# Kernel tuning notes

Hardware: AMD Instinct MI355X
Metric: run time of the kernel (lower is better)

## Reference

```python
import jax, jax.numpy as jnp
import numpy as np

N = 8192
F = 128

def setup_inputs() -> dict:
    key = jax.random.key(0)
    k1, k2, k3 = jax.random.split(key, 3)
    x = jax.random.normal(k1, (N, F), dtype=jnp.float32)
    adj = jax.random.uniform(k2, (N, N), dtype=jnp.float32)
    # xavier-uniform style init for weight [F, F]
    limit = float(np.sqrt(6.0 / (F + F)))
    weight = jax.random.uniform(k3, (F, F), dtype=jnp.float32, minval=-limit, maxval=limit)
    return {"x": x, "adj": adj, "weight": weight}

def reference(x, adj, weight):
    # adj_hat = adj + I
    n = adj.shape[0]
    adj_hat = adj + jnp.eye(n, dtype=adj.dtype)
    # degree vector; D^{-1/2} A_hat D^{-1/2} expressed as row/col scaling
    deg = jnp.sum(adj_hat, axis=1)
    d_inv_sqrt = (deg + 1e-8) ** -0.5  # [N]
    support = d_inv_sqrt[:, None] * adj_hat * d_inv_sqrt[None, :]  # [N, N]
    out = jnp.matmul(jnp.matmul(support, x), weight)  # [N, F]
    return jax.nn.relu(out)
```

## Files before the change

### kernel.cpp

```cpp
#include <hip/hip_runtime.h>
#include <hip/hip_bf16.h>

#define NN 8192
#define FF 128
#define BM 64
#define BK 64
#define KS 8
#define KCH (NN / KS)
#define NSTEP (KCH / BK)

typedef __attribute__((ext_vector_type(8))) short bf16x8;
typedef __attribute__((ext_vector_type(4))) float f32x4;

__device__ __forceinline__ short f2bf(float f) {
  unsigned u = __float_as_uint(f);
  u += 0x7FFFu + ((u >> 16) & 1u);
  return (short)(u >> 16);
}
__device__ __forceinline__ float bf2f(short s) {
  return __uint_as_float(((unsigned)(unsigned short)s) << 16);
}

__global__ __launch_bounds__(256) void k_deg(const float* __restrict__ adj,
                                             float* __restrict__ dinv) {
  const int row = blockIdx.x;
  const float4* p = (const float4*)(adj + (size_t)row * NN);
  float s = 0.f;
#pragma unroll
  for (int it = 0; it < 8; ++it) {
    float4 v = p[it * 256 + threadIdx.x];
    s += (v.x + v.y) + (v.z + v.w);
  }
#pragma unroll
  for (int off = 32; off > 0; off >>= 1) s += __shfl_down(s, off, 64);
  __shared__ float partial[4];
  if ((threadIdx.x & 63) == 0) partial[threadIdx.x >> 6] = s;
  __syncthreads();
  if (threadIdx.x == 0) {
    float deg = (partial[0] + partial[1]) + (partial[2] + partial[3]) + 1.0f;
    dinv[row] = 1.0f / sqrtf(deg + 1e-8f);
  }
}

__global__ __launch_bounds__(256) void k_scale_t(const float* __restrict__ x,
                                                 const float* __restrict__ dinv,
                                                 short* __restrict__ yT) {
  __shared__ float tile[64][129];
  const int r0 = blockIdx.x * 64;
  const int tid = threadIdx.x;
#pragma unroll
  for (int it = 0; it < 8; ++it) {
    int q = it * 256 + tid;
    int r = q >> 5;
    int c = q & 31;
    float4 v = ((const float4*)(x + (size_t)(r0 + r) * FF))[c];
    float d = dinv[r0 + r];
    tile[r][c * 4 + 0] = v.x * d;
    tile[r][c * 4 + 1] = v.y * d;
    tile[r][c * 4 + 2] = v.z * d;
    tile[r][c * 4 + 3] = v.w * d;
  }
  __syncthreads();
  const int f = tid >> 1;
  const int i0 = (tid & 1) * 32;
#pragma unroll
  for (int g = 0; g < 4; ++g) {
    bf16x8 o;
#pragma unroll
    for (int j = 0; j < 8; ++j) o[j] = f2bf(tile[i0 + g * 8 + j][f]);
    *(bf16x8*)(yT + (size_t)f * NN + r0 + i0 + g * 8) = o;
  }
}

__global__ __launch_bounds__(512, 4) void k_gemm(const float* __restrict__ adj,
                                                 const short* __restrict__ yT,
                                                 short* __restrict__ zpart) {
  __shared__ short As[2][BM][72];
  __shared__ short Bs[2][128][72];
  const int tid = threadIdx.x;
  const int wave = tid >> 6;
  const int lane = tid & 63;
  const int mb = 127 - (int)(blockIdx.x & 127);
  const int ks = blockIdx.x >> 7;
  const int row0 = mb * BM;
  const size_t kbase = (size_t)ks * KCH;

  const int s_ar = tid >> 3;
  const int s_ac = (tid & 7) * 8;
  const float* pa  = adj + (size_t)(row0 + s_ar) * NN + kbase + s_ac;
  const short* pb0 = yT + (size_t)s_ar * NN + kbase + s_ac;
  const short* pb1 = yT + (size_t)(s_ar + 64) * NN + kbase + s_ac;

  const int wm = (wave >> 2) * 32;
  const int wn = (wave & 3) * 32;
  const int fr = lane & 15;
  const int kh = (lane >> 4) * 8;

  f32x4 acc00 = {0.f,0.f,0.f,0.f}, acc01 = acc00, acc10 = acc00, acc11 = acc00;

  float4 aXlo, aXhi, aYlo, aYhi;
  bf16x8 bX0, bX1, bY0, bY1;

#define LOADT(alo, ahi, b0v, b1v, koff) do {                                   \
    alo = *(const float4*)(pa + (koff));                                       \
    ahi = *(const float4*)(pa + (koff) + 4);                                   \
    b0v = *(const bf16x8*)(pb0 + (koff));                                      \
    b1v = *(const bf16x8*)(pb1 + (koff));                                      \
  } while (0)

#define STAGE(BUF, alo, ahi, b0v, b1v) do {                                    \
    bf16x8 ap_;                                                                \
    ap_[0] = f2bf(alo.x); ap_[1] = f2bf(alo.y);                                \
    ap_[2] = f2bf(alo.z); ap_[3] = f2bf(alo.w);                                \
    ap_[4] = f2bf(ahi.x); ap_[5] = f2bf(ahi.y);                                \
    ap_[6] = f2bf(ahi.z); ap_[7] = f2bf(ahi.w);                                \
    *(bf16x8*)&As[BUF][s_ar][s_ac] = ap_;                                      \
    *(bf16x8*)&Bs[BUF][s_ar][s_ac] = b0v;                                      \
    *(bf16x8*)&Bs[BUF][s_ar + 64][s_ac] = b1v;                                 \
  } while (0)

#define COMPUTE(BUF) do {                                                      \
    _Pragma("unroll")                                                          \
    for (int kk = 0; kk < 2; ++kk) {                                           \
      bf16x8 a0 = *(const bf16x8*)&As[BUF][wm + fr][kk * 32 + kh];             \
      bf16x8 a1 = *(const bf16x8*)&As[BUF][wm + 16 + fr][kk * 32 + kh];        \
      bf16x8 b0 = *(const bf16x8*)&Bs[BUF][wn + fr][kk * 32 + kh];             \
      bf16x8 b1 = *(const bf16x8*)&Bs[BUF][wn + 16 + fr][kk * 32 + kh];        \
      acc00 = __builtin_amdgcn_mfma_f32_16x16x32_bf16(a0, b0, acc00, 0, 0, 0); \
      acc01 = __builtin_amdgcn_mfma_f32_16x16x32_bf16(a0, b1, acc01, 0, 0, 0); \
      acc10 = __builtin_amdgcn_mfma_f32_16x16x32_bf16(a1, b0, acc10, 0, 0, 0); \
      acc11 = __builtin_amdgcn_mfma_f32_16x16x32_bf16(a1, b1, acc11, 0, 0, 0); \
    }                                                                          \
  } while (0)

  LOADT(aXlo, aXhi, bX0, bX1, 0);
  LOADT(aYlo, aYhi, bY0, bY1, BK);
  STAGE(0, aXlo, aXhi, bX0, bX1);
  __syncthreads();

  for (int step = 0; step < NSTEP; step += 2) {
    STAGE(1, aYlo, aYhi, bY0, bY1);
    if (step + 2 < NSTEP) LOADT(aXlo, aXhi, bX0, bX1, (step + 2) * BK);
    COMPUTE(0);
    __syncthreads();
    if (step + 2 < NSTEP) STAGE(0, aXlo, aXhi, bX0, bX1);
    if (step + 3 < NSTEP) LOADT(aYlo, aYhi, bY0, bY1, (step + 3) * BK);
    COMPUTE(1);
    __syncthreads();
  }

  const int r4 = (lane >> 4) * 4;
  short* zp = zpart + ((size_t)ks << 20);
#pragma unroll
  for (int r = 0; r < 4; ++r) {
    int gi0 = row0 + wm + r4 + r;
    int gi1 = gi0 + 16;
    zp[(size_t)gi0 * FF + wn + fr]      = f2bf(acc00[r]);
    zp[(size_t)gi0 * FF + wn + 16 + fr] = f2bf(acc01[r]);
    zp[(size_t)gi1 * FF + wn + fr]      = f2bf(acc10[r]);
    zp[(size_t)gi1 * FF + wn + 16 + fr] = f2bf(acc11[r]);
  }
#undef LOADT
#undef STAGE
#undef COMPUTE
}

__global__ __launch_bounds__(256) void k_out(const short* __restrict__ zpart,
                                             const float* __restrict__ x,
                                             const float* __restrict__ dinv,
                                             const float* __restrict__ w,
                                             float* __restrict__ out) {
  __shared__ float zs[16][128];
  const int r0 = blockIdx.x * 16;
  const int tid = threadIdx.x;
#pragma unroll
  for (int half = 0; half < 2; ++half) {
    int p = half * 256 + tid;
    int r = p >> 5;
    int c4 = p & 31;
    int gi = r0 + r;
    const short* base = zpart + (size_t)gi * FF + c4 * 4;
    float s0 = 0.f, s1 = 0.f, s2 = 0.f, s3 = 0.f;
#pragma unroll
    for (int sidx = 0; sidx < KS; ++sidx) {
      short4 v = *(const short4*)(base + ((size_t)sidx << 20));
      s0 += bf2f(v.x); s1 += bf2f(v.y); s2 += bf2f(v.z); s3 += bf2f(v.w);
    }
    float4 xv = *(const float4*)(x + (size_t)gi * FF + c4 * 4);
    float di = dinv[gi];
    float di2 = di * di;
    zs[r][c4 * 4 + 0] = di * s0 + di2 * xv.x;
    zs[r][c4 * 4 + 1] = di * s1 + di2 * xv.y;
    zs[r][c4 * 4 + 2] = di * s2 + di2 * xv.z;
    zs[r][c4 * 4 + 3] = di * s3 + di2 * xv.w;
  }
  __syncthreads();
  const int f = tid & 127;
  const int rg = (tid >> 7) * 8;
  float acc[8] = {0.f, 0.f, 0.f, 0.f, 0.f, 0.f, 0.f, 0.f};
#pragma unroll 4
  for (int k = 0; k < 128; ++k) {
    float wv = w[k * FF + f];
#pragma unroll
    for (int r = 0; r < 8; ++r) acc[r] += zs[rg + r][k] * wv;
  }
#pragma unroll
  for (int r = 0; r < 8; ++r) {
    out[(size_t)(r0 + rg + r) * FF + f] = fmaxf(acc[r], 0.0f);
  }
}

extern "C" void kernel_launch(void* const* d_in, const int* in_sizes, int n_in,
                              void* d_out, int out_size, void* d_ws, size_t ws_size,
                              hipStream_t stream) {
  const float* x   = (const float*)d_in[0];
  const float* adj = (const float*)d_in[1];
  const float* w   = (const float*)d_in[2];
  float* out = (float*)d_out;

  float* dinv  = (float*)d_ws;
  short* yT    = (short*)((char*)d_ws + 64 * 1024);
  short* zpart = (short*)((char*)d_ws + 4 * 1024 * 1024);

  k_deg    <<<NN,      256, 0, stream>>>(adj, dinv);
  k_scale_t<<<NN / 64, 256, 0, stream>>>(x, dinv, yT);
  k_gemm   <<<128 * KS, 512, 0, stream>>>(adj, yT, zpart);
  k_out    <<<NN / 16, 256, 0, stream>>>(zpart, x, dinv, w, out);
}
```

Baseline: 114.4 us.

## Double GEMM M-tile and load B operand directly into registers

The main GEMM now uses 128-row tiles, so each wave computes a 64x32 output with eight accumulators, and the grid shrinks to 512 blocks. The B operand (the scaled transposed features) is no longer staged through shared memory. Each wave loads its MFMA fragments straight from global memory into registers, double-buffered across steps. This halves the number of times the bf16 feature matrix is re-read per row block and removes the B shared-memory traffic. In exchange it costs more registers per thread, fewer blocks for the 256-CU device to occupy, and uncoalesced per-lane B loads.

```diff
diff --git a/kernel.cpp b/kernel.cpp
--- a/kernel.cpp
+++ b/kernel.cpp
@@ -3,7 +3,7 @@
 
 #define NN 8192
 #define FF 128
-#define BM 64
+#define BM 128
 #define BK 64
 #define KS 8
 #define KCH (NN / KS)
@@ -76,91 +76,115 @@
                                                  const short* __restrict__ yT,
                                                  short* __restrict__ zpart) {
   __shared__ short As[2][BM][72];
-  __shared__ short Bs[2][128][72];
   const int tid = threadIdx.x;
   const int wave = tid >> 6;
   const int lane = tid & 63;
-  const int mb = 127 - (int)(blockIdx.x & 127);
-  const int ks = blockIdx.x >> 7;
+  const int mb = 63 - (int)(blockIdx.x & 63);
+  const int ks = blockIdx.x >> 6;
   const int row0 = mb * BM;
   const size_t kbase = (size_t)ks * KCH;
 
-  const int s_ar = tid >> 3;
-  const int s_ac = (tid & 7) * 8;
-  const float* pa  = adj + (size_t)(row0 + s_ar) * NN + kbase + s_ac;
-  const short* pb0 = yT + (size_t)s_ar * NN + kbase + s_ac;
-  const short* pb1 = yT + (size_t)(s_ar + 64) * NN + kbase + s_ac;
-
-  const int wm = (wave >> 2) * 32;
+  const int s_ar = tid >> 2;
+  const int s_ac = (tid & 3) * 16;
+  const float* pa = adj + (size_t)(row0 + s_ar) * NN + kbase + s_ac;
+
+  const int wm = (wave >> 2) * 64;
   const int wn = (wave & 3) * 32;
   const int fr = lane & 15;
   const int kh = (lane >> 4) * 8;
 
+  const short* pb0 = yT + (size_t)(wn + fr) * NN + kbase + kh;
+  const short* pb1 = pb0 + (size_t)16 * NN;
+
   f32x4 acc00 = {0.f,0.f,0.f,0.f}, acc01 = acc00, acc10 = acc00, acc11 = acc00;
-
-  float4 aXlo, aXhi, aYlo, aYhi;
-  bf16x8 bX0, bX1, bY0, bY1;
-
-#define LOADT(alo, ahi, b0v, b1v, koff) do {                                   \
-    alo = *(const float4*)(pa + (koff));                                       \
-    ahi = *(const float4*)(pa + (koff) + 4);                                   \
-    b0v = *(const bf16x8*)(pb0 + (koff));                                      \
-    b1v = *(const bf16x8*)(pb1 + (koff));                                      \
-  } while (0)
-
-#define STAGE(BUF, alo, ahi, b0v, b1v) do {                                    \
-    bf16x8 ap_;                                                                \
-    ap_[0] = f2bf(alo.x); ap_[1] = f2bf(alo.y);                                \
-    ap_[2] = f2bf(alo.z); ap_[3] = f2bf(alo.w);                                \
-    ap_[4] = f2bf(ahi.x); ap_[5] = f2bf(ahi.y);                                \
-    ap_[6] = f2bf(ahi.z); ap_[7] = f2bf(ahi.w);                                \
-    *(bf16x8*)&As[BUF][s_ar][s_ac] = ap_;                                      \
-    *(bf16x8*)&Bs[BUF][s_ar][s_ac] = b0v;                                      \
-    *(bf16x8*)&Bs[BUF][s_ar + 64][s_ac] = b1v;                                 \
-  } while (0)
-
-#define COMPUTE(BUF) do {                                                      \
+  f32x4 acc20 = acc00, acc21 = acc00, acc30 = acc00, acc31 = acc00;
+
+  float4 aR0, aR1, aR2, aR3;
+  bf16x8 bX[4], bY[4];
+
+#define LOADA(koff) do {                                                       \
+    aR0 = *(const float4*)(pa + (koff));                                       \
+    aR1 = *(const float4*)(pa + (koff) + 4);                                   \
+    aR2 = *(const float4*)(pa + (koff) + 8);                                   \
+    aR3 = *(const float4*)(pa + (koff) + 12);                                  \
+  } while (0)
+
+#define LOADB(dst, koff) do {                                                  \
+    dst[0] = *(const bf16x8*)(pb0 + (koff));                                   \
+    dst[1] = *(const bf16x8*)(pb0 + (koff) + 32);                              \
+    dst[2] = *(const bf16x8*)(pb1 + (koff));                                   \
+    dst[3] = *(const bf16x8*)(pb1 + (koff) + 32);                              \
+  } while (0)
+
+#define STAGE(BUF) do {                                                        \
+    bf16x8 lo_, hi_;                                                           \
+    lo_[0] = f2bf(aR0.x); lo_[1] = f2bf(aR0.y);                                \
+    lo_[2] = f2bf(aR0.z); lo_[3] = f2bf(aR0.w);                                \
+    lo_[4] = f2bf(aR1.x); lo_[5] = f2bf(aR1.y);                                \
+    lo_[6] = f2bf(aR1.z); lo_[7] = f2bf(aR1.w);                                \
+    hi_[0] = f2bf(aR2.x); hi_[1] = f2bf(aR2.y);                                \
+    hi_[2] = f2bf(aR2.z); hi_[3] = f2bf(aR2.w);                                \
+    hi_[4] = f2bf(aR3.x); hi_[5] = f2bf(aR3.y);                                \
+    hi_[6] = f2bf(aR3.z); hi_[7] = f2bf(aR3.w);                                \
+    *(bf16x8*)&As[BUF][s_ar][s_ac]     = lo_;                                  \
+    *(bf16x8*)&As[BUF][s_ar][s_ac + 8] = hi_;                                  \
+  } while (0)
+
+#define COMPUTE(BUF, breg) do {                                                \
     _Pragma("unroll")                                                          \
     for (int kk = 0; kk < 2; ++kk) {                                           \
-      bf16x8 a0 = *(const bf16x8*)&As[BUF][wm + fr][kk * 32 + kh];             \
+      bf16x8 a0 = *(const bf16x8*)&As[BUF][wm +  0 + fr][kk * 32 + kh];        \
       bf16x8 a1 = *(const bf16x8*)&As[BUF][wm + 16 + fr][kk * 32 + kh];        \
-      bf16x8 b0 = *(const bf16x8*)&Bs[BUF][wn + fr][kk * 32 + kh];             \
-      bf16x8 b1 = *(const bf16x8*)&Bs[BUF][wn + 16 + fr][kk * 32 + kh];        \
-      acc00 = __builtin_amdgcn_mfma_f32_16x16x32_bf16(a0, b0, acc00, 0, 0, 0); \
-      acc01 = __builtin_amdgcn_mfma_f32_16x16x32_bf16(a0, b1, acc01, 0, 0, 0); \
-      acc10 = __builtin_amdgcn_mfma_f32_16x16x32_bf16(a1, b0, acc10, 0, 0, 0); \
-      acc11 = __builtin_amdgcn_mfma_f32_16x16x32_bf16(a1, b1, acc11, 0, 0, 0); \
+      bf16x8 a2 = *(const bf16x8*)&As[BUF][wm + 32 + fr][kk * 32 + kh];        \
+      bf16x8 a3 = *(const bf16x8*)&As[BUF][wm + 48 + fr][kk * 32 + kh];        \
+      acc00 = __builtin_amdgcn_mfma_f32_16x16x32_bf16(a0, breg[kk],     acc00, 0, 0, 0); \
+      acc01 = __builtin_amdgcn_mfma_f32_16x16x32_bf16(a0, breg[2 + kk], acc01, 0, 0, 0); \
+      acc10 = __builtin_amdgcn_mfma_f32_16x16x32_bf16(a1, breg[kk],     acc10, 0, 0, 0); \
+      acc11 = __builtin_amdgcn_mfma_f32_16x16x32_bf16(a1, breg[2 + kk], acc11, 0, 0, 0); \
+      acc20 = __builtin_amdgcn_mfma_f32_16x16x32_bf16(a2, breg[kk],     acc20, 0, 0, 0); \
+      acc21 = __builtin_amdgcn_mfma_f32_16x16x32_bf16(a2, breg[2 + kk], acc21, 0, 0, 0); \
+      acc30 = __builtin_amdgcn_mfma_f32_16x16x32_bf16(a3, breg[kk],     acc30, 0, 0, 0); \
+      acc31 = __builtin_amdgcn_mfma_f32_16x16x32_bf16(a3, breg[2 + kk], acc31, 0, 0, 0); \
     }                                                                          \
   } while (0)
 
-  LOADT(aXlo, aXhi, bX0, bX1, 0);
-  LOADT(aYlo, aYhi, bY0, bY1, BK);
-  STAGE(0, aXlo, aXhi, bX0, bX1);
+  LOADA(0);
+  STAGE(0);
+  LOADA(BK);
+  LOADB(bX, 0);
+  LOADB(bY, BK);
   __syncthreads();
 
   for (int step = 0; step < NSTEP; step += 2) {
-    STAGE(1, aYlo, aYhi, bY0, bY1);
-    if (step + 2 < NSTEP) LOADT(aXlo, aXhi, bX0, bX1, (step + 2) * BK);
-    COMPUTE(0);
+    if (step + 1 < NSTEP) STAGE(1);
+    if (step + 2 < NSTEP) LOADA((step + 2) * BK);
+    COMPUTE(0, bX);
+    if (step + 2 < NSTEP) LOADB(bX, (step + 2) * BK);
     __syncthreads();
-    if (step + 2 < NSTEP) STAGE(0, aXlo, aXhi, bX0, bX1);
-    if (step + 3 < NSTEP) LOADT(aYlo, aYhi, bY0, bY1, (step + 3) * BK);
-    COMPUTE(1);
+    if (step + 2 < NSTEP) STAGE(0);
+    if (step + 3 < NSTEP) LOADA((step + 3) * BK);
+    COMPUTE(1, bY);
+    if (step + 3 < NSTEP) LOADB(bY, (step + 3) * BK);
     __syncthreads();
   }
 
   const int r4 = (lane >> 4) * 4;
   short* zp = zpart + ((size_t)ks << 20);
-#pragma unroll
-  for (int r = 0; r < 4; ++r) {
-    int gi0 = row0 + wm + r4 + r;
-    int gi1 = gi0 + 16;
-    zp[(size_t)gi0 * FF + wn + fr]      = f2bf(acc00[r]);
-    zp[(size_t)gi0 * FF + wn + 16 + fr] = f2bf(acc01[r]);
-    zp[(size_t)gi1 * FF + wn + fr]      = f2bf(acc10[r]);
-    zp[(size_t)gi1 * FF + wn + 16 + fr] = f2bf(acc11[r]);
-  }
-#undef LOADT
+#define STOREM(accn0, accn1, MOFF) do {                                        \
+    _Pragma("unroll")                                                          \
+    for (int r = 0; r < 4; ++r) {                                              \
+      int gi = row0 + wm + (MOFF) + r4 + r;                                    \
+      zp[(size_t)gi * FF + wn + fr]      = f2bf(accn0[r]);                     \
+      zp[(size_t)gi * FF + wn + 16 + fr] = f2bf(accn1[r]);                     \
+    }                                                                          \
+  } while (0)
+  STOREM(acc00, acc01, 0);
+  STOREM(acc10, acc11, 16);
+  STOREM(acc20, acc21, 32);
+  STOREM(acc30, acc31, 48);
+#undef STOREM
+#undef LOADA
+#undef LOADB
 #undef STAGE
 #undef COMPUTE
 }
@@ -224,6 +248,6 @@
 
   k_deg    <<<NN,      256, 0, stream>>>(adj, dinv);
   k_scale_t<<<NN / 64, 256, 0, stream>>>(x, dinv, yT);
-  k_gemm   <<<128 * KS, 512, 0, stream>>>(adj, yT, zpart);
+  k_gemm   <<<64 * KS, 512, 0, stream>>>(adj, yT, zpart);
   k_out    <<<NN / 16, 256, 0, stream>>>(zpart, x, dinv, w, out);
 }
```

After: 120.6 us. +5.5%, slower.

## Stage GEMM tiles via direct global-to-LDS DMA with XOR swizzle

Applied to the files above, without the earlier changes.

The GEMM kernel now loads adjacency (fp32) and yT tiles straight from global memory into LDS with global_load_lds, so staging no longer passes through registers. A uses an XOR-swizzled layout to avoid bank conflicts. The fp32-to-bf16 conversion moves from staging to the compute phase and uses packed v_cvt_pk_bf16_f32. The fp32 A tile doubles LDS usage and the conversion is repeated by every wave that reads the tile; the occupancy hint in launch_bounds is also removed.

```diff
diff --git a/kernel.cpp b/kernel.cpp
--- a/kernel.cpp
+++ b/kernel.cpp
@@ -19,6 +19,22 @@
 }
 __device__ __forceinline__ float bf2f(short s) {
   return __uint_as_float(((unsigned)(unsigned short)s) << 16);
+}
+
+__device__ __forceinline__ void dma16(const void* g, void* lds) {
+  __builtin_amdgcn_global_load_lds(
+      (const __attribute__((address_space(1))) unsigned int*)(uintptr_t)g,
+      (__attribute__((address_space(3))) unsigned int*)(lds),
+      16, 0, 0);
+}
+
+__device__ __forceinline__ bf16x8 cvt8(float4 lo, float4 hi) {
+  union { bf16x8 v; unsigned u[4]; } r;
+  asm("v_cvt_pk_bf16_f32 %0, %1, %2" : "=v"(r.u[0]) : "v"(lo.x), "v"(lo.y));
+  asm("v_cvt_pk_bf16_f32 %0, %1, %2" : "=v"(r.u[1]) : "v"(lo.z), "v"(lo.w));
+  asm("v_cvt_pk_bf16_f32 %0, %1, %2" : "=v"(r.u[2]) : "v"(hi.x), "v"(hi.y));
+  asm("v_cvt_pk_bf16_f32 %0, %1, %2" : "=v"(r.u[3]) : "v"(hi.z), "v"(hi.w));
+  return r.v;
 }
 
 __global__ __launch_bounds__(256) void k_deg(const float* __restrict__ adj,
@@ -72,11 +88,11 @@
   }
 }
 
-__global__ __launch_bounds__(512, 4) void k_gemm(const float* __restrict__ adj,
-                                                 const short* __restrict__ yT,
-                                                 short* __restrict__ zpart) {
-  __shared__ short As[2][BM][72];
-  __shared__ short Bs[2][128][72];
+__global__ __launch_bounds__(512) void k_gemm(const float* __restrict__ adj,
+                                              const short* __restrict__ yT,
+                                              short* __restrict__ zpart) {
+  __shared__ float Asf[2][BM * BK];
+  __shared__ short Bsf[2][128 * BK];
   const int tid = threadIdx.x;
   const int wave = tid >> 6;
   const int lane = tid & 63;
@@ -85,47 +101,53 @@
   const int row0 = mb * BM;
   const size_t kbase = (size_t)ks * KCH;
 
-  const int s_ar = tid >> 3;
-  const int s_ac = (tid & 7) * 8;
-  const float* pa  = adj + (size_t)(row0 + s_ar) * NN + kbase + s_ac;
-  const short* pb0 = yT + (size_t)s_ar * NN + kbase + s_ac;
-  const short* pb1 = yT + (size_t)(s_ar + 64) * NN + kbase + s_ac;
+  const int rowA = tid >> 4;
+  const int c4l  = (tid & 15) ^ (rowA & 7);
+  const float* pa0 = adj + (size_t)(row0 + rowA) * NN + kbase + c4l * 4;
+  const float* pa1 = pa0 + (size_t)32 * NN;
+  const int rowB = tid >> 3;
+  const int c8l  = (tid & 7) ^ (rowB & 7);
+  const short* pb0 = yT + (size_t)rowB * NN + kbase + c8l * 8;
+  const short* pb1 = pb0 + (size_t)64 * NN;
+
+  const int ldsOff = wave * 1024;
+
+#define STAGE_DMA(BUF, koff) do {                                              \
+    char* la = (char*)&Asf[BUF][0] + ldsOff;                                   \
+    char* lb = (char*)&Bsf[BUF][0] + ldsOff;                                   \
+    dma16(pa0 + (koff), la);                                                   \
+    dma16(pa1 + (koff), la + 8192);                                            \
+    dma16(pb0 + (koff), lb);                                                   \
+    dma16(pb1 + (koff), lb + 8192);                                            \
+  } while (0)
 
   const int wm = (wave >> 2) * 32;
   const int wn = (wave & 3) * 32;
   const int fr = lane & 15;
   const int kh = (lane >> 4) * 8;
+  const int khq = kh >> 2;
+  const int kh8 = kh >> 3;
+  const int sw  = fr & 7;
+  const int ra0 = wm + fr, ra1 = ra0 + 16;
+  const int rb0 = wn + fr, rb1 = rb0 + 16;
 
   f32x4 acc00 = {0.f,0.f,0.f,0.f}, acc01 = acc00, acc10 = acc00, acc11 = acc00;
 
-  float4 aXlo, aXhi, aYlo, aYhi;
-  bf16x8 bX0, bX1, bY0, bY1;
-
-#define LOADT(alo, ahi, b0v, b1v, koff) do {                                   \
-    alo = *(const float4*)(pa + (koff));                                       \
-    ahi = *(const float4*)(pa + (koff) + 4);                                   \
-    b0v = *(const bf16x8*)(pb0 + (koff));                                      \
-    b1v = *(const bf16x8*)(pb1 + (koff));                                      \
-  } while (0)
-
-#define STAGE(BUF, alo, ahi, b0v, b1v) do {                                    \
-    bf16x8 ap_;                                                                \
-    ap_[0] = f2bf(alo.x); ap_[1] = f2bf(alo.y);                                \
-    ap_[2] = f2bf(alo.z); ap_[3] = f2bf(alo.w);                                \
-    ap_[4] = f2bf(ahi.x); ap_[5] = f2bf(ahi.y);                                \
-    ap_[6] = f2bf(ahi.z); ap_[7] = f2bf(ahi.w);                                \
-    *(bf16x8*)&As[BUF][s_ar][s_ac] = ap_;                                      \
-    *(bf16x8*)&Bs[BUF][s_ar][s_ac] = b0v;                                      \
-    *(bf16x8*)&Bs[BUF][s_ar + 64][s_ac] = b1v;                                 \
-  } while (0)
-
 #define COMPUTE(BUF) do {                                                      \
+    const char* Ab = (const char*)&Asf[BUF][0];                                \
+    const char* Bb = (const char*)&Bsf[BUF][0];                                \
     _Pragma("unroll")                                                          \
     for (int kk = 0; kk < 2; ++kk) {                                           \
-      bf16x8 a0 = *(const bf16x8*)&As[BUF][wm + fr][kk * 32 + kh];             \
-      bf16x8 a1 = *(const bf16x8*)&As[BUF][wm + 16 + fr][kk * 32 + kh];        \
-      bf16x8 b0 = *(const bf16x8*)&Bs[BUF][wn + fr][kk * 32 + kh];             \
-      bf16x8 b1 = *(const bf16x8*)&Bs[BUF][wn + 16 + fr][kk * 32 + kh];        \
+      int c4 = kk * 8 + khq;                                                   \
+      int c8 = kk * 4 + kh8;                                                   \
+      float4 lo0 = *(const float4*)(Ab + ra0 * 256 + (((c4    ) ^ sw) << 4));  \
+      float4 hi0 = *(const float4*)(Ab + ra0 * 256 + (((c4 + 1) ^ sw) << 4));  \
+      float4 lo1 = *(const float4*)(Ab + ra1 * 256 + (((c4    ) ^ sw) << 4));  \
+      float4 hi1 = *(const float4*)(Ab + ra1 * 256 + (((c4 + 1) ^ sw) << 4));  \
+      bf16x8 b0 = *(const bf16x8*)(Bb + rb0 * 128 + ((c8 ^ sw) << 4));         \
+      bf16x8 b1 = *(const bf16x8*)(Bb + rb1 * 128 + ((c8 ^ sw) << 4));         \
+      bf16x8 a0 = cvt8(lo0, hi0);                                              \
+      bf16x8 a1 = cvt8(lo1, hi1);                                              \
       acc00 = __builtin_amdgcn_mfma_f32_16x16x32_bf16(a0, b0, acc00, 0, 0, 0); \
       acc01 = __builtin_amdgcn_mfma_f32_16x16x32_bf16(a0, b1, acc01, 0, 0, 0); \
       acc10 = __builtin_amdgcn_mfma_f32_16x16x32_bf16(a1, b0, acc10, 0, 0, 0); \
@@ -133,20 +155,16 @@
     }                                                                          \
   } while (0)
 
-  LOADT(aXlo, aXhi, bX0, bX1, 0);
-  LOADT(aYlo, aYhi, bY0, bY1, BK);
-  STAGE(0, aXlo, aXhi, bX0, bX1);
-  __syncthreads();
-
-  for (int step = 0; step < NSTEP; step += 2) {
-    STAGE(1, aYlo, aYhi, bY0, bY1);
-    if (step + 2 < NSTEP) LOADT(aXlo, aXhi, bX0, bX1, (step + 2) * BK);
-    COMPUTE(0);
+  STAGE_DMA(0, 0);
+  __syncthreads();
+
+  int buf = 0;
+  for (int t = 0; t < NSTEP; ++t) {
+    if (t + 1 < NSTEP) STAGE_DMA(buf ^ 1, (t + 1) * BK);
+    __builtin_amdgcn_sched_barrier(0);
+    COMPUTE(buf);
     __syncthreads();
-    if (step + 2 < NSTEP) STAGE(0, aXlo, aXhi, bX0, bX1);
-    if (step + 3 < NSTEP) LOADT(aYlo, aYhi, bY0, bY1, (step + 3) * BK);
-    COMPUTE(1);
-    __syncthreads();
+    buf ^= 1;
   }
 
   const int r4 = (lane >> 4) * 4;
@@ -160,8 +178,7 @@
     zp[(size_t)gi1 * FF + wn + fr]      = f2bf(acc10[r]);
     zp[(size_t)gi1 * FF + wn + 16 + fr] = f2bf(acc11[r]);
   }
-#undef LOADT
-#undef STAGE
+#undef STAGE_DMA
 #undef COMPUTE
 }
 
@@ -222,8 +239,8 @@
   short* yT    = (short*)((char*)d_ws + 64 * 1024);
   short* zpart = (short*)((char*)d_ws + 4 * 1024 * 1024);
 
-  k_deg    <<<NN,      256, 0, stream>>>(adj, dinv);
-  k_scale_t<<<NN / 64, 256, 0, stream>>>(x, dinv, yT);
+  k_deg    <<<NN,       256, 0, stream>>>(adj, dinv);
+  k_scale_t<<<NN / 64,  256, 0, stream>>>(x, dinv, yT);
   k_gemm   <<<128 * KS, 512, 0, stream>>>(adj, yT, zpart);
-  k_out    <<<NN / 16, 256, 0, stream>>>(zpart, x, dinv, w, out);
-}
+  k_out    <<<NN / 16,  256, 0, stream>>>(zpart, x, dinv, w, out);
+}
```

Result: no change. 113.0 us, median of 2 (-1.2%).
